# Kernel tuning notes

Hardware: AMD Instinct MI355X
Metric: run time of the kernel (lower is better)

The kernel has to match this reference:

```python
import jax, jax.numpy as jnp
import numpy as np

B, L, D, C, H, NB = 2, 2048, 256, 8, 8, 2
S = 2                        # spatial coord dim of s
E = 2 * D - (C + 1)          # id-embedding width per D*2-(C+1)
FIN = 1 + S + E + C          # z + s + id-embed + conditionals
MAXLOC = 4096
DH = (2 * D) // H            # per-head dim


def _ln(x, sc, b):
    m = x.mean(-1, keepdims=True)
    v = ((x - m) ** 2).mean(-1, keepdims=True)
    return (x - m) * jax.lax.rsqrt(v + 1e-6) * sc + b


def setup_inputs() -> dict:
    key = jax.random.key(0)
    ks = iter(jax.random.split(key, 64))
    nrm = lambda shape: jax.random.normal(next(ks), shape, jnp.float32) * 0.02
    inp = {
        "z": jax.random.normal(next(ks), (B, L), jnp.float32),
        "conditionals": jax.random.normal(next(ks), (C,), jnp.float32),
        "s": jax.random.uniform(next(ks), (L, S), jnp.float32),
        "K": jax.random.uniform(next(ks), (L, L), jnp.float32),
        "embed": nrm((MAXLOC, E)),
        "W_in1": nrm((FIN, 4 * D)), "b_in1": jnp.zeros((4 * D,), jnp.float32),
        "W_in2": nrm((4 * D, D)), "b_in2": jnp.zeros((D,), jnp.float32),
        "bias_w": jnp.ones((NB,), jnp.float32), "bias_b": jnp.zeros((NB,), jnp.float32),
        "Wq": nrm((NB, D, 2 * D)), "bq": jnp.zeros((NB, 2 * D), jnp.float32),
        "Wk": nrm((NB, D, 2 * D)), "bk": jnp.zeros((NB, 2 * D), jnp.float32),
        "Wv": nrm((NB, D, 2 * D)), "bv": jnp.zeros((NB, 2 * D), jnp.float32),
        "Wo": nrm((NB, 2 * D, D)), "bo": jnp.zeros((NB, D), jnp.float32),
        "ln1_s": jnp.ones((NB, D), jnp.float32), "ln1_b": jnp.zeros((NB, D), jnp.float32),
        "ln2_s": jnp.ones((NB, D), jnp.float32), "ln2_b": jnp.zeros((NB, D), jnp.float32),
        "Wf1": nrm((NB, D, 4 * D)), "bf1": jnp.zeros((NB, 4 * D), jnp.float32),
        "Wf2": nrm((NB, 4 * D, D)), "bf2": jnp.zeros((NB, D), jnp.float32),
        "Wh1": nrm((D, 128)), "bh1": jnp.zeros((128,), jnp.float32),
        "Wh2": nrm((128, 1)), "bh2": jnp.zeros((1,), jnp.float32),
    }
    return inp


def reference(z, conditionals, s, K, embed, W_in1, b_in1, W_in2, b_in2,
              bias_w, bias_b, Wq, bq, Wk, bk, Wv, bv, Wo, bo,
              ln1_s, ln1_b, ln2_s, ln2_b, Wf1, bf1, Wf2, bf2,
              Wh1, bh1, Wh2, bh2):
    Bx, Lx = z.shape
    ids_e = embed[:Lx]  # ids = arange(L), so embedding lookup is a leading slice
    feats = jnp.concatenate([
        z[..., None],                                          # (B, L, 1)
        jnp.broadcast_to(s[None], (Bx, Lx, S)),                # (B, L, S)
        jnp.broadcast_to(ids_e[None], (Bx, Lx, E)),            # (B, L, E)
        jnp.broadcast_to(conditionals[None, None], (Bx, Lx, C)),  # cond_as_feats
    ], axis=-1)
    x = jax.nn.gelu(feats @ W_in1 + b_in1) @ W_in2 + b_in2     # (B, L, D)
    for i in range(NB):
        bias = bias_w[i] * K + bias_b[i]                        # learned scalar-affine kernel bias (L, L)
        h = _ln(x, ln1_s[i], ln1_b[i])
        q = (h @ Wq[i] + bq[i]).reshape(Bx, Lx, H, DH)
        k = (h @ Wk[i] + bk[i]).reshape(Bx, Lx, H, DH)
        v = (h @ Wv[i] + bv[i]).reshape(Bx, Lx, H, DH)
        scores = jnp.einsum('bqhd,bkhd->bhqk', q, k) / jnp.sqrt(jnp.float32(DH))
        scores = scores + bias[None, None]                      # broadcast over batch, heads
        a = jax.nn.softmax(scores, axis=-1)
        o = jnp.einsum('bhqk,bkhd->bqhd', a, v).reshape(Bx, Lx, 2 * D)
        x = x + (o @ Wo[i] + bo[i])
        h2 = _ln(x, ln2_s[i], ln2_b[i])
        x = x + jax.nn.gelu(h2 @ Wf1[i] + bf1[i]) @ Wf2[i] + bf2[i]
    return jax.nn.gelu(x @ Wh1 + bh1) @ Wh2 + bh2              # head MLP([128,1]) -> (B, L, 1)
```

## Files before the change

kernel.cpp:

```cpp
#include <hip/hip_runtime.h>
#include <math.h>

#define B_SZ 2
#define L_LEN 2048
#define D_MOD 256
#define H_HEADS 8
#define NB_BLK 2
#define S_SZ 2
#define E_SZ 503
#define C_SZ 8
#define FIN 514
#define FIN_PAD 576
#define LOG2E 1.44269504088896340736f
#define QSC (0.125f * LOG2E)

typedef short bf16x8 __attribute__((ext_vector_type(8)));
typedef float f32x4 __attribute__((ext_vector_type(4)));
typedef unsigned short u16x4 __attribute__((ext_vector_type(4)));
typedef unsigned short u16x8 __attribute__((ext_vector_type(8)));

#define OFF_IN1 0
#define OFF_IN2 589824
#define OFF_QKV 851968
#define OFF_O   1638400
#define OFF_F1  1900544
#define OFF_F2  2424832
#define OFF_H   2949120
#define WT_END  3047424

__device__ __forceinline__ unsigned short f2bf(float x) {
    unsigned u = __float_as_uint(x);
    u += 0x7FFFu + ((u >> 16) & 1u);
    return (unsigned short)(u >> 16);
}

__device__ __forceinline__ float bf2f(unsigned short h) {
    return __uint_as_float(((unsigned)h) << 16);
}

__device__ __forceinline__ float gelu_f(float x) {
    float x3 = x * x * x;
    return 0.5f * x * (1.0f + tanhf(0.7978845608028654f * (x + 0.044715f * x3)));
}

__device__ __forceinline__ void gll16(const void* g, void* l) {
    __builtin_amdgcn_global_load_lds(
        (const __attribute__((address_space(1))) unsigned int*)g,
        (__attribute__((address_space(3))) unsigned int*)l,
        16, 0, 0);
}

__global__ __launch_bounds__(256) void prep_kernel(
    const float* __restrict__ W_in1, const float* __restrict__ W_in2,
    const float* __restrict__ Wq, const float* __restrict__ Wk,
    const float* __restrict__ Wv, const float* __restrict__ Wo,
    const float* __restrict__ Wf1, const float* __restrict__ Wf2,
    const float* __restrict__ Wh1, const float* __restrict__ Kmat,
    const float* __restrict__ bias_w,
    const float* __restrict__ bq, const float* __restrict__ bk,
    const float* __restrict__ bv,
    const float* __restrict__ z, const float* __restrict__ s,
    const float* __restrict__ embed, const float* __restrict__ cond,
    unsigned short* __restrict__ wt, unsigned short* __restrict__ kbt,
    float* __restrict__ bqkv, unsigned short* __restrict__ feats)
{
    __shared__ float sTf[64][65];
    int b = blockIdx.x;
    int t = threadIdx.x;

    if (b < 720) {
        unsigned short (*sT)[65] = (unsigned short (*)[65])&sTf[0][0];
        const float* src; unsigned short* dst; int K, N, Kp, tile;
        float scale = 1.0f;
        if (b < 144)      { src = W_in1; dst = wt + OFF_IN1; K = 514;  N = 1024; Kp = 576;  tile = b; }
        else if (b < 208) { src = W_in2; dst = wt + OFF_IN2; K = 1024; N = 256;  Kp = 1024; tile = b - 144; }
        else if (b < 400) { int t2 = b - 208;
                            int sec = t2 >> 5; tile = t2 & 31;
                            int i = sec / 3, which = sec % 3;
                            const float* wsrc = which == 0 ? Wq : which == 1 ? Wk : Wv;
                            if (which == 0) scale = QSC;
                            src = wsrc + (size_t)i * 131072;
                            dst = wt + OFF_QKV + (size_t)i * 393216 + (size_t)which * 131072;
                            K = 256; N = 512; Kp = 256; }
        else if (b < 464) { int t2 = b - 400; int i = t2 >> 5; tile = t2 & 31;
                            src = Wo + (size_t)i * 131072; dst = wt + OFF_O + (size_t)i * 131072;
                            K = 512; N = 256; Kp = 512; }
        else if (b < 592) { int t2 = b - 464; int i = t2 >> 6; tile = t2 & 63;
                            src = Wf1 + (size_t)i * 262144; dst = wt + OFF_F1 + (size_t)i * 262144;
                            K = 256; N = 1024; Kp = 256; }
        else              { int t2 = b - 592; int i = t2 >> 6; tile = t2 & 63;
                            src = Wf2 + (size_t)i * 262144; dst = wt + OFF_F2 + (size_t)i * 262144;
                            K = 1024; N = 256; Kp = 1024; }

        int nt = N >> 6;
        int kt0 = (tile / nt) << 6;
        int nt0 = (tile % nt) << 6;
        #pragma unroll
        for (int p = 0; p < 4; p++) {
            int r = p * 16 + (t >> 4);
            int c = (t & 15) * 4;
            float4 v4 = make_float4(0.f, 0.f, 0.f, 0.f);
            if (kt0 + r < K) v4 = *(const float4*)(src + (size_t)(kt0 + r) * N + nt0 + c);
            sT[r][c + 0] = f2bf(v4.x * scale);
            sT[r][c + 1] = f2bf(v4.y * scale);
            sT[r][c + 2] = f2bf(v4.z * scale);
            sT[r][c + 3] = f2bf(v4.w * scale);
        }
        __syncthreads();
        int n = t >> 2, kq = (t & 3) * 16;
        u16x8 o0, o1;
        #pragma unroll
        for (int j = 0; j < 8; j++) {
            o0[j] = sT[kq + j][n];
            o1[j] = sT[kq + 8 + j][n];
        }
        unsigned short* dp = dst + (size_t)(nt0 + n) * Kp + kt0 + kq;
        *(u16x8*)(dp) = o0;
        *(u16x8*)(dp + 8) = o1;
    } else if (b < 1104) {
        int idx = (b - 720) * 256 + t;
        if (idx < 128 * 768) {
            int n = idx / 768, kk = idx % 768;
            int kz = kk & 255;
            float v = Wh1[(size_t)kz * 128 + n];
            unsigned short hi = f2bf(v);
            wt[OFF_H + idx] = (kk < 512) ? hi : f2bf(v - bf2f(hi));
        }
    } else if (b < 2128) {
        int tile = b - 1104;
        int qt0 = (tile & 31) << 6, kt0 = (tile >> 5) << 6;
        int rr = t >> 4, cc = (t & 15) << 2;
        #pragma unroll
        for (int p = 0; p < 4; p++) {
            int qr = p * 16 + rr;
            float4 v4 = *(const float4*)(Kmat + (size_t)(qt0 + qr) * L_LEN + kt0 + cc);
            sTf[cc + 0][qr] = v4.x;
            sTf[cc + 1][qr] = v4.y;
            sTf[cc + 2][qr] = v4.z;
            sTf[cc + 3][qr] = v4.w;
        }
        __syncthreads();
        float s0 = bias_w[0] * LOG2E, s1 = bias_w[1] * LOG2E;
        int kr = t >> 2, qc = (t & 3) << 4;
        u16x8 a0, a1, b0, b1;
        #pragma unroll
        for (int j = 0; j < 8; j++) {
            float v = sTf[kr][qc + j];
            a0[j] = f2bf(v * s0); b0[j] = f2bf(v * s1);
            float v2 = sTf[kr][qc + 8 + j];
            a1[j] = f2bf(v2 * s0); b1[j] = f2bf(v2 * s1);
        }
        unsigned short* d0 = kbt + (size_t)(kt0 + kr) * L_LEN + qt0 + qc;
        *(u16x8*)d0 = a0; *(u16x8*)(d0 + 8) = a1;
        unsigned short* d1 = d0 + (size_t)L_LEN * L_LEN;
        *(u16x8*)d1 = b0; *(u16x8*)(d1 + 8) = b1;
    } else if (b < 2140) {
        int idx = (b - 2128) * 256 + t;
        if (idx < 2 * 1536) {
            int i = idx / 1536, c = idx % 1536;
            float v;
            if (c < 512)       v = bq[i * 512 + c] * QSC;
            else if (c < 1024) v = bk[i * 512 + c - 512];
            else               v = bv[i * 512 + c - 1024];
            bqkv[idx] = v;
        }
    } else {
        int idx = (b - 2140) * 256 + t;
        const int total = B_SZ * L_LEN * FIN_PAD;
        if (idx < total) {
            int f = idx % FIN_PAD;
            int row = idx / FIN_PAD;
            int l = row % L_LEN;
            float val;
            if (f == 0)                   val = z[row];
            else if (f < 1 + S_SZ)        val = s[l * S_SZ + (f - 1)];
            else if (f < 1 + S_SZ + E_SZ) val = embed[(size_t)l * E_SZ + (f - 3)];
            else if (f < FIN)             val = cond[f - (1 + S_SZ + E_SZ)];
            else                          val = 0.0f;
            feats[idx] = f2bf(val);
        }
    }
}

__global__ __launch_bounds__(256) void xsplit_kernel(
    const float* __restrict__ x, unsigned short* __restrict__ xb)
{
    int t = blockIdx.x * 256 + threadIdx.x;
    int row = t >> 5, c8 = (t & 31) * 8;
    const float* xr = x + (size_t)row * 256 + c8;
    float4 a = *(const float4*)(xr);
    float4 b4 = *(const float4*)(xr + 4);
    u16x8 hi = { f2bf(a.x), f2bf(a.y), f2bf(a.z), f2bf(a.w),
                 f2bf(b4.x), f2bf(b4.y), f2bf(b4.z), f2bf(b4.w) };
    u16x8 lo = { f2bf(a.x - bf2f(hi[0])), f2bf(a.y - bf2f(hi[1])),
                 f2bf(a.z - bf2f(hi[2])), f2bf(a.w - bf2f(hi[3])),
                 f2bf(b4.x - bf2f(hi[4])), f2bf(b4.y - bf2f(hi[5])),
                 f2bf(b4.z - bf2f(hi[6])), f2bf(b4.w - bf2f(hi[7])) };
    unsigned short* orow = xb + (size_t)row * 768;
    *(u16x8*)(orow + c8) = hi;
    *(u16x8*)(orow + 256 + c8) = lo;
    *(u16x8*)(orow + 512 + c8) = hi;
}

template<int ACT, int OMODE>
__global__ __launch_bounds__(256) void gemmW(
    const unsigned short* __restrict__ A, const unsigned short* __restrict__ Wt,
    const float* __restrict__ bias, unsigned short* __restrict__ Cb,
    unsigned short* __restrict__ Cbk, unsigned short* __restrict__ Cbv,
    int M, int N, int Kd, int lda)
{
    __shared__ unsigned short sA[2][64][64];
    __shared__ unsigned short sB[2][128][64];
    const int tid = threadIdx.x;
    const int l = tid & 63, w = tid >> 6;
    const int g = l >> 4, n16 = l & 15;
    const int wr = w >> 1, wc = w & 1;
    const int m0 = blockIdx.y * 64, n0 = blockIdx.x * 128;
    const int r8 = l >> 3;
    const int swz8 = ((l & 7) ^ r8) * 8;

    f32x4 acc[2][4];
    #pragma unroll
    for (int mi = 0; mi < 2; mi++)
        #pragma unroll
        for (int ni = 0; ni < 4; ni++)
            acc[mi][ni] = (f32x4){0.f, 0.f, 0.f, 0.f};

#define STAGEW(buf, k0)                                                         \
    do {                                                                        \
        _Pragma("unroll")                                                       \
        for (int p = 0; p < 2; p++) {                                           \
            int row = w * 16 + p * 8 + r8;                                      \
            gll16(A + (size_t)(m0 + row) * lda + (k0) + swz8,                   \
                  &sA[buf][w * 16 + p * 8][0]);                                 \
        }                                                                       \
        _Pragma("unroll")                                                       \
        for (int p = 0; p < 4; p++) {                                           \
            int row = w * 32 + p * 8 + r8;                                      \
            gll16(Wt + (size_t)(n0 + row) * Kd + (k0) + swz8,                   \
                  &sB[buf][w * 32 + p * 8][0]);                                 \
        }                                                                       \
    } while (0)

    STAGEW(0, 0);
    __syncthreads();

    int cur = 0;
    for (int k0 = 0; k0 < Kd; k0 += 64) {
        int nxt = cur ^ 1;
        if (k0 + 64 < Kd) STAGEW(nxt, k0 + 64);
        #pragma unroll
        for (int ks = 0; ks < 2; ks++) {
            bf16x8 af[2], bfr[4];
            #pragma unroll
            for (int mi = 0; mi < 2; mi++) {
                int row = wr * 32 + mi * 16 + n16;
                af[mi] = *(const bf16x8*)((const char*)&sA[cur][row][0]
                          + ((ks * 64 + g * 16) ^ ((n16 & 7) << 4)));
            }
            #pragma unroll
            for (int ni = 0; ni < 4; ni++) {
                int row = wc * 64 + ni * 16 + n16;
                bfr[ni] = *(const bf16x8*)((const char*)&sB[cur][row][0]
                          + ((ks * 64 + g * 16) ^ ((n16 & 7) << 4)));
            }
            #pragma unroll
            for (int mi = 0; mi < 2; mi++)
                #pragma unroll
                for (int ni = 0; ni < 4; ni++)
                    acc[mi][ni] = __builtin_amdgcn_mfma_f32_16x16x32_bf16(
                        af[mi], bfr[ni], acc[mi][ni], 0, 0, 0);
        }
        __syncthreads();
        cur = nxt;
    }
#undef STAGEW

    #pragma unroll
    for (int mi = 0; mi < 2; mi++) {
        #pragma unroll
        for (int ni = 0; ni < 4; ni++) {
            int col = n0 + wc * 64 + ni * 16 + n16;
            float bv = bias[col];
            #pragma unroll
            for (int r = 0; r < 4; r++) {
                int row = m0 + wr * 32 + mi * 16 + 4 * g + r;
                float val = acc[mi][ni][r] + bv;
                if (ACT == 1) val = gelu_f(val);
                if (OMODE == 1) {
                    Cb[(size_t)row * N + col] = f2bf(val);
                } else {
                    if (col < 1024) {
                        unsigned short* dst = (col < 512) ? Cb : Cbk;
                        dst[(size_t)row * 512 + (col & 511)] = f2bf(val);
                    } else {
                        Cbv[((size_t)(row >> 11) * 512 + (col - 1024)) * L_LEN + (row & (L_LEN - 1))] = f2bf(val);
                    }
                }
            }
        }
    }
}

template<int ACT, int OMODE, int BM>
__global__ __launch_bounds__(256) void gemm_bf16(
    const unsigned short* __restrict__ A, const unsigned short* __restrict__ Wt,
    const float* __restrict__ bias, float* __restrict__ Cf,
    unsigned short* __restrict__ Cb, int M, int N, int Kd, int lda)
{
    __shared__ unsigned short sA[2][BM][64];
    __shared__ unsigned short sB[2][64][64];
    const int tid = threadIdx.x;
    const int l = tid & 63, w = tid >> 6;
    const int g = l >> 4, n16 = l & 15;
    const int m0 = blockIdx.y * BM, n0 = blockIdx.x * 64;

    const int r8 = l >> 3;
    const int swz8 = ((l & 7) ^ r8) * 8;

    const int NMI = (BM == 64) ? 2 : 1;
    const int wr = w >> 1;
    const int wc = w & 1;

    f32x4 acc[2][2];
    #pragma unroll
    for (int mi = 0; mi < 2; mi++)
        #pragma unroll
        for (int ni = 0; ni < 2; ni++)
            acc[mi][ni] = (f32x4){0.f, 0.f, 0.f, 0.f};

#define STAGE(buf, k0)                                                          \
    do {                                                                        \
        if (BM == 64) {                                                         \
            _Pragma("unroll")                                                   \
            for (int p = 0; p < 2; p++) {                                       \
                int row = w * 16 + p * 8 + r8;                                  \
                gll16(A + (size_t)(m0 + row) * lda + (k0) + swz8,               \
                      &sA[buf][w * 16 + p * 8][0]);                             \
            }                                                                   \
        } else {                                                                \
            int row = w * 8 + r8;                                               \
            gll16(A + (size_t)(m0 + row) * lda + (k0) + swz8,                   \
                  &sA[buf][w * 8][0]);                                          \
        }                                                                       \
        _Pragma("unroll")                                                       \
        for (int p = 0; p < 2; p++) {                                           \
            int row = w * 16 + p * 8 + r8;                                      \
            gll16(Wt + (size_t)(n0 + row) * Kd + (k0) + swz8,                   \
                  &sB[buf][w * 16 + p * 8][0]);                                 \
        }                                                                       \
    } while (0)

    STAGE(0, 0);
    __syncthreads();

    int cur = 0;
    for (int k0 = 0; k0 < Kd; k0 += 64) {
        int nxt = cur ^ 1;
        if (k0 + 64 < Kd) STAGE(nxt, k0 + 64);
        #pragma unroll
        for (int ks = 0; ks < 2; ks++) {
            bf16x8 af[2], bfr[2];
            #pragma unroll
            for (int mi = 0; mi < NMI; mi++) {
                int row = (BM == 64) ? (wr * 32 + mi * 16 + n16) : (wr * 16 + n16);
                af[mi] = *(const bf16x8*)((const char*)&sA[cur][row][0]
                          + ((ks * 64 + g * 16) ^ ((n16 & 7) << 4)));
            }
            #pragma unroll
            for (int ni = 0; ni < 2; ni++) {
                int row = wc * 32 + ni * 16 + n16;
                bfr[ni] = *(const bf16x8*)((const char*)&sB[cur][row][0]
                          + ((ks * 64 + g * 16) ^ ((n16 & 7) << 4)));
            }
            #pragma unroll
            for (int mi = 0; mi < NMI; mi++)
                #pragma unroll
                for (int ni = 0; ni < 2; ni++)
                    acc[mi][ni] = __builtin_amdgcn_mfma_f32_16x16x32_bf16(
                        af[mi], bfr[ni], acc[mi][ni], 0, 0, 0);
        }
        __syncthreads();
        cur = nxt;
    }
#undef STAGE

    #pragma unroll
    for (int mi = 0; mi < NMI; mi++) {
        #pragma unroll
        for (int ni = 0; ni < 2; ni++) {
            int col = n0 + wc * 32 + ni * 16 + n16;
            float bv = bias[col];
            #pragma unroll
            for (int r = 0; r < 4; r++) {
                int row = (BM == 64) ? (m0 + wr * 32 + mi * 16 + 4 * g + r)
                                     : (m0 + wr * 16 + 4 * g + r);
                float val = acc[mi][ni][r] + bv;
                if (ACT == 1) val = gelu_f(val);
                if (OMODE == 0) {
                    Cf[(size_t)row * N + col] = val;
                } else if (OMODE == 1) {
                    Cb[(size_t)row * N + col] = f2bf(val);
                } else {
                    float* cp = Cf + (size_t)row * N + col;
                    *cp += val;
                }
            }
        }
    }
}

__global__ __launch_bounds__(256) void ln_bf16(
    const float* __restrict__ x, const float* __restrict__ sc,
    const float* __restrict__ bi, unsigned short* __restrict__ out)
{
    int wave = threadIdx.x >> 6, lane = threadIdx.x & 63;
    int row = blockIdx.x * 4 + wave;
    const float* xr = x + (size_t)row * D_MOD;
    float4 v = *(const float4*)(xr + lane * 4);
    float s1 = v.x + v.y + v.z + v.w;
    float s2 = v.x * v.x + v.y * v.y + v.z * v.z + v.w * v.w;
    #pragma unroll
    for (int off = 1; off < 64; off <<= 1) {
        s1 += __shfl_xor(s1, off);
        s2 += __shfl_xor(s2, off);
    }
    float mean = s1 * (1.0f / 256.0f);
    float var = s2 * (1.0f / 256.0f) - mean * mean;
    float rs = rsqrtf(var + 1e-6f);
    float4 scv = *(const float4*)(sc + lane * 4);
    float4 bv  = *(const float4*)(bi + lane * 4);
    u16x4 o4;
    o4[0] = f2bf((v.x - mean) * rs * scv.x + bv.x);
    o4[1] = f2bf((v.y - mean) * rs * scv.y + bv.y);
    o4[2] = f2bf((v.z - mean) * rs * scv.z + bv.z);
    o4[3] = f2bf((v.w - mean) * rs * scv.w + bv.w);
    *(u16x4*)(out + (size_t)row * D_MOD + lane * 4) = o4;
}

__global__ __launch_bounds__(256, 2) void attn_mfma(
    const unsigned short* __restrict__ q, const unsigned short* __restrict__ k,
    const unsigned short* __restrict__ vt, const unsigned short* __restrict__ kmt,
    unsigned short* __restrict__ o)
{
    __shared__ unsigned short sK[2][64][64];
    __shared__ unsigned short sV[2][64][64];
    __shared__ unsigned short sKmT[2][64][64];
    __shared__ unsigned short sP[4][16][72];

    const int tid = threadIdx.x;
    const int l = tid & 63, w = tid >> 6;
    const int g = l >> 4, n16 = l & 15;
    const int qblk = blockIdx.x * 64, hh = blockIdx.y, b = blockIdx.z;

    const int r8 = l >> 3;
    const int swz8 = ((l & 7) ^ r8) * 8;

    bf16x8 qf[2];
    {
        const unsigned short* qp = q + (size_t)(b * L_LEN + qblk + w * 16 + n16) * 512 + hh * 64;
        qf[0] = *(const bf16x8*)(qp + g * 8);
        qf[1] = *(const bf16x8*)(qp + 32 + g * 8);
    }
    bf16x8 onesf;
    #pragma unroll
    for (int j = 0; j < 8; j++) onesf[j] = (short)0x3F80;

    f32x4 o_acc[4];
    #pragma unroll
    for (int c = 0; c < 4; c++) o_acc[c] = (f32x4){0.f, 0.f, 0.f, 0.f};
    f32x4 l_acc = (f32x4){0.f, 0.f, 0.f, 0.f};

    const unsigned short* kbase = k + (size_t)b * L_LEN * 512 + hh * 64;
    const unsigned short* vbase = vt + ((size_t)b * 512 + hh * 64) * L_LEN;

    #pragma unroll
    for (int p = 0; p < 2; p++) {
        int row = w * 16 + p * 8 + r8;
        gll16(kbase + (size_t)row * 512 + swz8, &sK[0][w * 16 + p * 8][0]);
        gll16(vbase + (size_t)row * L_LEN + swz8, &sV[0][w * 16 + p * 8][0]);
        gll16(kmt + (size_t)row * L_LEN + qblk + swz8, &sKmT[0][w * 16 + p * 8][0]);
    }
    __syncthreads();

    int cur = 0;
    for (int kt = 0; kt < L_LEN / 64; kt++) {
        const int nb = cur ^ 1;
        const int kblk2 = (kt + 1) << 6;
        if (kt + 1 < L_LEN / 64) {
            #pragma unroll
            for (int p = 0; p < 2; p++) {
                int row = w * 16 + p * 8 + r8;
                gll16(kbase + (size_t)(kblk2 + row) * 512 + swz8, &sK[nb][w * 16 + p * 8][0]);
                gll16(vbase + (size_t)row * L_LEN + kblk2 + swz8, &sV[nb][w * 16 + p * 8][0]);
                gll16(kmt + (size_t)(kblk2 + row) * L_LEN + qblk + swz8, &sKmT[nb][w * 16 + p * 8][0]);
            }
        }
        f32x4 sacc[4];
        #pragma unroll
        for (int c = 0; c < 4; c++) {
            const char* kb_ = (const char*)&sKmT[cur][c * 16 + n16][0];
            u16x4 kmv = *(const u16x4*)(kb_ + ((32 * w + 8 * g) ^ ((n16 & 7) << 4)));
            #pragma unroll
            for (int r = 0; r < 4; r++)
                sacc[c][r] = bf2f((unsigned short)kmv[r]);
        }
        __builtin_amdgcn_s_setprio(1);
        #pragma unroll
        for (int ks = 0; ks < 2; ks++)
            #pragma unroll
            for (int c = 0; c < 4; c++) {
                int row = c * 16 + n16;
                bf16x8 kf = *(const bf16x8*)((const char*)&sK[cur][row][0]
                             + ((ks * 64 + g * 16) ^ ((n16 & 7) << 4)));
                sacc[c] = __builtin_amdgcn_mfma_f32_16x16x32_bf16(qf[ks], kf, sacc[c], 0, 0, 0);
            }
        __builtin_amdgcn_s_setprio(0);
        float p[4][4];
        #pragma unroll
        for (int r = 0; r < 4; r++)
            #pragma unroll
            for (int c = 0; c < 4; c++)
                p[r][c] = __builtin_amdgcn_exp2f(sacc[c][r]);
        #pragma unroll
        for (int r = 0; r < 4; r++)
            #pragma unroll
            for (int c = 0; c < 4; c++)
                sP[w][4 * g + r][c * 16 + n16] = f2bf(p[r][c]);
        __builtin_amdgcn_s_setprio(1);
        #pragma unroll
        for (int ks = 0; ks < 2; ks++) {
            bf16x8 pf = *(const bf16x8*)&sP[w][n16][ks * 32 + g * 8];
            l_acc = __builtin_amdgcn_mfma_f32_16x16x32_bf16(pf, onesf, l_acc, 0, 0, 0);
            #pragma unroll
            for (int c = 0; c < 4; c++) {
                int row = c * 16 + n16;
                bf16x8 vf = *(const bf16x8*)((const char*)&sV[cur][row][0]
                             + ((ks * 64 + g * 16) ^ ((n16 & 7) << 4)));
                o_acc[c] = __builtin_amdgcn_mfma_f32_16x16x32_bf16(pf, vf, o_acc[c], 0, 0, 0);
            }
        }
        __builtin_amdgcn_s_setprio(0);
        __syncthreads();
        cur = nb;
    }

    float inv[4];
    #pragma unroll
    for (int r = 0; r < 4; r++) inv[r] = 1.0f / l_acc[r];
    #pragma unroll
    for (int c = 0; c < 4; c++)
        #pragma unroll
        for (int r = 0; r < 4; r++)
            o[(size_t)(b * L_LEN + qblk + w * 16 + 4 * g + r) * 512 + hh * 64 + c * 16 + n16]
                = f2bf(o_acc[c][r] * inv[r]);
}

__global__ __launch_bounds__(256) void hsum_kernel(
    const unsigned short* __restrict__ hb, const float* __restrict__ Wh2,
    const float* __restrict__ bh2, float* __restrict__ out)
{
    int wave = threadIdx.x >> 6, lane = threadIdx.x & 63;
    int row = blockIdx.x * 4 + wave;
    unsigned v = *(const unsigned*)(hb + (size_t)row * 128 + lane * 2);
    float v0 = __uint_as_float((v & 0xFFFFu) << 16);
    float v1 = __uint_as_float(v & 0xFFFF0000u);
    float val = v0 * Wh2[lane * 2] + v1 * Wh2[lane * 2 + 1];
    #pragma unroll
    for (int off = 1; off < 64; off <<= 1)
        val += __shfl_xor(val, off);
    if (lane == 0) out[row] = val + bh2[0];
}

extern "C" void kernel_launch(void* const* d_in, const int* in_sizes, int n_in,
                              void* d_out, int out_size, void* d_ws, size_t ws_size,
                              hipStream_t stream)
{
    const float* z      = (const float*)d_in[0];
    const float* cond   = (const float*)d_in[1];
    const float* s      = (const float*)d_in[2];
    const float* Kmat   = (const float*)d_in[3];
    const float* embed  = (const float*)d_in[4];
    const float* W_in1  = (const float*)d_in[5];
    const float* b_in1  = (const float*)d_in[6];
    const float* W_in2  = (const float*)d_in[7];
    const float* b_in2  = (const float*)d_in[8];
    const float* bias_w = (const float*)d_in[9];
    const float* bias_b = (const float*)d_in[10];
    const float* Wq     = (const float*)d_in[11];
    const float* bq     = (const float*)d_in[12];
    const float* Wk     = (const float*)d_in[13];
    const float* bk     = (const float*)d_in[14];
    const float* Wv     = (const float*)d_in[15];
    const float* bv     = (const float*)d_in[16];
    const float* Wo     = (const float*)d_in[17];
    const float* bo     = (const float*)d_in[18];
    const float* ln1_s  = (const float*)d_in[19];
    const float* ln1_b  = (const float*)d_in[20];
    const float* ln2_s  = (const float*)d_in[21];
    const float* ln2_b  = (const float*)d_in[22];
    const float* Wf1    = (const float*)d_in[23];
    const float* bf1    = (const float*)d_in[24];
    const float* Wf2    = (const float*)d_in[25];
    const float* bf2    = (const float*)d_in[26];
    const float* Wh1    = (const float*)d_in[27];
    const float* bh1    = (const float*)d_in[28];
    const float* Wh2    = (const float*)d_in[29];
    const float* bh2    = (const float*)d_in[30];
    float* out = (float*)d_out;
    (void)bias_b;

    const int M = B_SZ * L_LEN;
    char* base = (char*)d_ws;
    unsigned short* feats = (unsigned short*)base;
    float* x = (float*)(base + (size_t)M * FIN_PAD * 2);
    unsigned short* h    = (unsigned short*)((char*)x + (size_t)M * D_MOD * 4);
    unsigned short* hid1 = h    + (size_t)M * D_MOD;
    unsigned short* qb   = hid1 + (size_t)M * 1024;
    unsigned short* kb2  = qb   + (size_t)M * 512;
    unsigned short* vtb  = kb2  + (size_t)M * 512;
    unsigned short* ob   = vtb  + (size_t)M * 512;
    unsigned short* wt   = ob   + (size_t)M * 512;
    float* bqkv          = (float*)(wt + WT_END);
    unsigned short* kbt  = (unsigned short*)(bqkv + 2 * 1536);

    prep_kernel<<<dim3(11356), dim3(256), 0, stream>>>(
        W_in1, W_in2, Wq, Wk, Wv, Wo, Wf1, Wf2, Wh1, Kmat, bias_w,
        bq, bk, bv, z, s, embed, cond, wt, kbt, bqkv, feats);

    gemmW<1, 1><<<dim3(8, 64), 256, 0, stream>>>(feats, wt + OFF_IN1, b_in1, hid1, nullptr, nullptr, M, 1024, FIN_PAD, FIN_PAD);
    gemm_bf16<0, 0, 32><<<dim3(4, 128), 256, 0, stream>>>(hid1, wt + OFF_IN2, b_in2, x, nullptr, M, 256, 1024, 1024);

    for (int i = 0; i < NB_BLK; i++) {
        ln_bf16<<<dim3(M / 4), 256, 0, stream>>>(x, ln1_s + i * D_MOD, ln1_b + i * D_MOD, h);
        gemmW<0, 4><<<dim3(12, 64), 256, 0, stream>>>(h, wt + OFF_QKV + (size_t)i * 393216, bqkv + i * 1536, qb, kb2, vtb, M, 1536, 256, 256);
        attn_mfma<<<dim3(L_LEN / 64, H_HEADS, B_SZ), 256, 0, stream>>>(qb, kb2, vtb, kbt + (size_t)i * L_LEN * L_LEN, ob);
        gemm_bf16<0, 2, 32><<<dim3(4, 128), 256, 0, stream>>>(ob, wt + OFF_O + (size_t)i * 131072, bo + i * D_MOD, x, nullptr, M, 256, 512, 512);
        ln_bf16<<<dim3(M / 4), 256, 0, stream>>>(x, ln2_s + i * D_MOD, ln2_b + i * D_MOD, h);
        gemmW<1, 1><<<dim3(8, 64), 256, 0, stream>>>(h, wt + OFF_F1 + (size_t)i * 262144, bf1 + i * 1024, hid1, nullptr, nullptr, M, 1024, 256, 256);
        gemm_bf16<0, 2, 32><<<dim3(4, 128), 256, 0, stream>>>(hid1, wt + OFF_F2 + (size_t)i * 262144, bf2 + i * D_MOD, x, nullptr, M, 256, 1024, 1024);
    }
    xsplit_kernel<<<dim3(512), dim3(256), 0, stream>>>(x, hid1);
    gemm_bf16<1, 1, 64><<<dim3(2, 64), 256, 0, stream>>>(hid1, wt + OFF_H, bh1, nullptr, qb, M, 128, 768, 768);
    hsum_kernel<<<dim3(M / 4), 256, 0, stream>>>(qb, Wh2, bh2, out);
}
```

Before: 247.9 us.

## Prelay kernel bias in MFMA fragment order and fuse x split into FFN GEMM

The prep kernel now writes the scaled kernel-bias matrix directly in per-thread MFMA accumulator fragment order, so the attention kernel loads it from global memory into registers (double-buffered across key tiles) instead of staging a transposed tile through LDS. This removes the sKmT shared buffer and its LDS reads, lowering LDS use and possibly raising occupancy. Separately, the last FFN down-projection GEMM gets a new output mode that adds the residual and emits the hi/lo bf16 split directly, removing the standalone xsplit kernel launch. Costs: more register pressure in attention and scattered scalar global reads in the prep stage.

```diff
diff --git a/kernel.cpp b/kernel.cpp
--- a/kernel.cpp
+++ b/kernel.cpp
@@ -61,15 +61,14 @@
     const float* __restrict__ bv,
     const float* __restrict__ z, const float* __restrict__ s,
     const float* __restrict__ embed, const float* __restrict__ cond,
-    unsigned short* __restrict__ wt, unsigned short* __restrict__ kbt,
+    unsigned short* __restrict__ wt, unsigned short* __restrict__ kmfrag,
     float* __restrict__ bqkv, unsigned short* __restrict__ feats)
 {
-    __shared__ float sTf[64][65];
+    __shared__ unsigned short sT[64][65];
     int b = blockIdx.x;
     int t = threadIdx.x;
 
     if (b < 720) {
-        unsigned short (*sT)[65] = (unsigned short (*)[65])&sTf[0][0];
         const float* src; unsigned short* dst; int K, N, Kp, tile;
         float scale = 1.0f;
         if (b < 144)      { src = W_in1; dst = wt + OFF_IN1; K = 514;  N = 1024; Kp = 576;  tile = b; }
@@ -126,36 +125,28 @@
             unsigned short hi = f2bf(v);
             wt[OFF_H + idx] = (kk < 512) ? hi : f2bf(v - bf2f(hi));
         }
-    } else if (b < 2128) {
-        int tile = b - 1104;
-        int qt0 = (tile & 31) << 6, kt0 = (tile >> 5) << 6;
-        int rr = t >> 4, cc = (t & 15) << 2;
-        #pragma unroll
-        for (int p = 0; p < 4; p++) {
-            int qr = p * 16 + rr;
-            float4 v4 = *(const float4*)(Kmat + (size_t)(qt0 + qr) * L_LEN + kt0 + cc);
-            sTf[cc + 0][qr] = v4.x;
-            sTf[cc + 1][qr] = v4.y;
-            sTf[cc + 2][qr] = v4.z;
-            sTf[cc + 3][qr] = v4.w;
-        }
-        __syncthreads();
-        float s0 = bias_w[0] * LOG2E, s1 = bias_w[1] * LOG2E;
-        int kr = t >> 2, qc = (t & 3) << 4;
-        u16x8 a0, a1, b0, b1;
-        #pragma unroll
-        for (int j = 0; j < 8; j++) {
-            float v = sTf[kr][qc + j];
-            a0[j] = f2bf(v * s0); b0[j] = f2bf(v * s1);
-            float v2 = sTf[kr][qc + 8 + j];
-            a1[j] = f2bf(v2 * s0); b1[j] = f2bf(v2 * s1);
-        }
-        unsigned short* d0 = kbt + (size_t)(kt0 + kr) * L_LEN + qt0 + qc;
-        *(u16x8*)d0 = a0; *(u16x8*)(d0 + 8) = a1;
-        unsigned short* d1 = d0 + (size_t)L_LEN * L_LEN;
-        *(u16x8*)d1 = b0; *(u16x8*)(d1 + 8) = b1;
-    } else if (b < 2140) {
-        int idx = (b - 2128) * 256 + t;
+    } else if (b < 3152) {
+        int t2 = b - 1104;
+        int i = t2 >> 10, rem = t2 & 1023;
+        int kt = rem >> 5, qb = rem & 31;
+        float sc = bias_w[i] * LOG2E;
+        int q0 = qb * 64 + ((t >> 6) << 4) + (((t >> 4) & 3) << 2);
+        int k0 = kt * 64 + (t & 15);
+        u16x8 f0, f1;
+        #pragma unroll
+        for (int c = 0; c < 4; c++)
+            #pragma unroll
+            for (int r = 0; r < 4; r++) {
+                float v = Kmat[(size_t)(q0 + r) * L_LEN + k0 + c * 16] * sc;
+                if (c < 2) f0[c * 4 + r] = f2bf(v);
+                else       f1[(c - 2) * 4 + r] = f2bf(v);
+            }
+        unsigned short* dp = kmfrag + ((size_t)i << 22)
+                           + (((size_t)(kt * 32 + qb)) * 256 + t) * 16;
+        *(u16x8*)dp = f0;
+        *(u16x8*)(dp + 8) = f1;
+    } else if (b < 3164) {
+        int idx = (b - 3152) * 256 + t;
         if (idx < 2 * 1536) {
             int i = idx / 1536, c = idx % 1536;
             float v;
@@ -165,7 +156,7 @@
             bqkv[idx] = v;
         }
     } else {
-        int idx = (b - 2140) * 256 + t;
+        int idx = (b - 3164) * 256 + t;
         const int total = B_SZ * L_LEN * FIN_PAD;
         if (idx < total) {
             int f = idx % FIN_PAD;
@@ -180,26 +171,6 @@
             feats[idx] = f2bf(val);
         }
     }
-}
-
-__global__ __launch_bounds__(256) void xsplit_kernel(
-    const float* __restrict__ x, unsigned short* __restrict__ xb)
-{
-    int t = blockIdx.x * 256 + threadIdx.x;
-    int row = t >> 5, c8 = (t & 31) * 8;
-    const float* xr = x + (size_t)row * 256 + c8;
-    float4 a = *(const float4*)(xr);
-    float4 b4 = *(const float4*)(xr + 4);
-    u16x8 hi = { f2bf(a.x), f2bf(a.y), f2bf(a.z), f2bf(a.w),
-                 f2bf(b4.x), f2bf(b4.y), f2bf(b4.z), f2bf(b4.w) };
-    u16x8 lo = { f2bf(a.x - bf2f(hi[0])), f2bf(a.y - bf2f(hi[1])),
-                 f2bf(a.z - bf2f(hi[2])), f2bf(a.w - bf2f(hi[3])),
-                 f2bf(b4.x - bf2f(hi[4])), f2bf(b4.y - bf2f(hi[5])),
-                 f2bf(b4.z - bf2f(hi[6])), f2bf(b4.w - bf2f(hi[7])) };
-    unsigned short* orow = xb + (size_t)row * 768;
-    *(u16x8*)(orow + c8) = hi;
-    *(u16x8*)(orow + 256 + c8) = lo;
-    *(u16x8*)(orow + 512 + c8) = hi;
 }
 
 template<int ACT, int OMODE>
@@ -401,9 +372,17 @@
                     Cf[(size_t)row * N + col] = val;
                 } else if (OMODE == 1) {
                     Cb[(size_t)row * N + col] = f2bf(val);
-                } else {
+                } else if (OMODE == 2) {
                     float* cp = Cf + (size_t)row * N + col;
                     *cp += val;
+                } else if (OMODE == 5) {
+                    float xnew = Cf[(size_t)row * N + col] + val;
+                    unsigned short hi = f2bf(xnew);
+                    unsigned short lo = f2bf(xnew - bf2f(hi));
+                    unsigned short* orow = Cb + (size_t)row * 768;
+                    orow[col] = hi;
+                    orow[256 + col] = lo;
+                    orow[512 + col] = hi;
                 }
             }
         }
@@ -440,12 +419,11 @@
 
 __global__ __launch_bounds__(256, 2) void attn_mfma(
     const unsigned short* __restrict__ q, const unsigned short* __restrict__ k,
-    const unsigned short* __restrict__ vt, const unsigned short* __restrict__ kmt,
+    const unsigned short* __restrict__ vt, const unsigned short* __restrict__ kmf,
     unsigned short* __restrict__ o)
 {
     __shared__ unsigned short sK[2][64][64];
     __shared__ unsigned short sV[2][64][64];
-    __shared__ unsigned short sKmT[2][64][64];
     __shared__ unsigned short sP[4][16][72];
 
     const int tid = threadIdx.x;
@@ -473,38 +451,40 @@
 
     const unsigned short* kbase = k + (size_t)b * L_LEN * 512 + hh * 64;
     const unsigned short* vbase = vt + ((size_t)b * 512 + hh * 64) * L_LEN;
+    const unsigned short* kmbase = kmf + ((size_t)blockIdx.x * 256 + tid) * 16;
 
     #pragma unroll
     for (int p = 0; p < 2; p++) {
         int row = w * 16 + p * 8 + r8;
         gll16(kbase + (size_t)row * 512 + swz8, &sK[0][w * 16 + p * 8][0]);
         gll16(vbase + (size_t)row * L_LEN + swz8, &sV[0][w * 16 + p * 8][0]);
-        gll16(kmt + (size_t)row * L_LEN + qblk + swz8, &sKmT[0][w * 16 + p * 8][0]);
-    }
+    }
+    u16x8 kmC0 = *(const u16x8*)kmbase;
+    u16x8 kmC1 = *(const u16x8*)(kmbase + 8);
     __syncthreads();
 
     int cur = 0;
     for (int kt = 0; kt < L_LEN / 64; kt++) {
         const int nb = cur ^ 1;
         const int kblk2 = (kt + 1) << 6;
+        u16x8 kmN0 = kmC0, kmN1 = kmC1;
         if (kt + 1 < L_LEN / 64) {
             #pragma unroll
             for (int p = 0; p < 2; p++) {
                 int row = w * 16 + p * 8 + r8;
                 gll16(kbase + (size_t)(kblk2 + row) * 512 + swz8, &sK[nb][w * 16 + p * 8][0]);
                 gll16(vbase + (size_t)row * L_LEN + kblk2 + swz8, &sV[nb][w * 16 + p * 8][0]);
-                gll16(kmt + (size_t)(kblk2 + row) * L_LEN + qblk + swz8, &sKmT[nb][w * 16 + p * 8][0]);
-            }
+            }
+            const unsigned short* kp2 = kmbase + (size_t)(kt + 1) * 131072;
+            kmN0 = *(const u16x8*)kp2;
+            kmN1 = *(const u16x8*)(kp2 + 8);
         }
         f32x4 sacc[4];
         #pragma unroll
-        for (int c = 0; c < 4; c++) {
-            const char* kb_ = (const char*)&sKmT[cur][c * 16 + n16][0];
-            u16x4 kmv = *(const u16x4*)(kb_ + ((32 * w + 8 * g) ^ ((n16 & 7) << 4)));
+        for (int c = 0; c < 4; c++)
             #pragma unroll
             for (int r = 0; r < 4; r++)
-                sacc[c][r] = bf2f((unsigned short)kmv[r]);
-        }
+                sacc[c][r] = bf2f((unsigned short)(c < 2 ? kmC0[c * 4 + r] : kmC1[(c - 2) * 4 + r]));
         __builtin_amdgcn_s_setprio(1);
         #pragma unroll
         for (int ks = 0; ks < 2; ks++)
@@ -543,6 +523,8 @@
         __builtin_amdgcn_s_setprio(0);
         __syncthreads();
         cur = nb;
+        kmC0 = kmN0;
+        kmC1 = kmN1;
     }
 
     float inv[4];
@@ -622,11 +604,11 @@
     unsigned short* ob   = vtb  + (size_t)M * 512;
     unsigned short* wt   = ob   + (size_t)M * 512;
     float* bqkv          = (float*)(wt + WT_END);
-    unsigned short* kbt  = (unsigned short*)(bqkv + 2 * 1536);
-
-    prep_kernel<<<dim3(11356), dim3(256), 0, stream>>>(
+    unsigned short* kmfrag = (unsigned short*)(bqkv + 2 * 1536);
+
+    prep_kernel<<<dim3(12380), dim3(256), 0, stream>>>(
         W_in1, W_in2, Wq, Wk, Wv, Wo, Wf1, Wf2, Wh1, Kmat, bias_w,
-        bq, bk, bv, z, s, embed, cond, wt, kbt, bqkv, feats);
+        bq, bk, bv, z, s, embed, cond, wt, kmfrag, bqkv, feats);
 
     gemmW<1, 1><<<dim3(8, 64), 256, 0, stream>>>(feats, wt + OFF_IN1, b_in1, hid1, nullptr, nullptr, M, 1024, FIN_PAD, FIN_PAD);
     gemm_bf16<0, 0, 32><<<dim3(4, 128), 256, 0, stream>>>(hid1, wt + OFF_IN2, b_in2, x, nullptr, M, 256, 1024, 1024);
@@ -634,13 +616,15 @@
     for (int i = 0; i < NB_BLK; i++) {
         ln_bf16<<<dim3(M / 4), 256, 0, stream>>>(x, ln1_s + i * D_MOD, ln1_b + i * D_MOD, h);
         gemmW<0, 4><<<dim3(12, 64), 256, 0, stream>>>(h, wt + OFF_QKV + (size_t)i * 393216, bqkv + i * 1536, qb, kb2, vtb, M, 1536, 256, 256);
-        attn_mfma<<<dim3(L_LEN / 64, H_HEADS, B_SZ), 256, 0, stream>>>(qb, kb2, vtb, kbt + (size_t)i * L_LEN * L_LEN, ob);
+        attn_mfma<<<dim3(L_LEN / 64, H_HEADS, B_SZ), 256, 0, stream>>>(qb, kb2, vtb, kmfrag + ((size_t)i << 22), ob);
         gemm_bf16<0, 2, 32><<<dim3(4, 128), 256, 0, stream>>>(ob, wt + OFF_O + (size_t)i * 131072, bo + i * D_MOD, x, nullptr, M, 256, 512, 512);
         ln_bf16<<<dim3(M / 4), 256, 0, stream>>>(x, ln2_s + i * D_MOD, ln2_b + i * D_MOD, h);
         gemmW<1, 1><<<dim3(8, 64), 256, 0, stream>>>(h, wt + OFF_F1 + (size_t)i * 262144, bf1 + i * 1024, hid1, nullptr, nullptr, M, 1024, 256, 256);
-        gemm_bf16<0, 2, 32><<<dim3(4, 128), 256, 0, stream>>>(hid1, wt + OFF_F2 + (size_t)i * 262144, bf2 + i * D_MOD, x, nullptr, M, 256, 1024, 1024);
-    }
-    xsplit_kernel<<<dim3(512), dim3(256), 0, stream>>>(x, hid1);
-    gemm_bf16<1, 1, 64><<<dim3(2, 64), 256, 0, stream>>>(hid1, wt + OFF_H, bh1, nullptr, qb, M, 128, 768, 768);
-    hsum_kernel<<<dim3(M / 4), 256, 0, stream>>>(qb, Wh2, bh2, out);
-}
+        if (i == 0)
+            gemm_bf16<0, 2, 32><<<dim3(4, 128), 256, 0, stream>>>(hid1, wt + OFF_F2 + (size_t)i * 262144, bf2 + i * D_MOD, x, nullptr, M, 256, 1024, 1024);
+        else
+            gemm_bf16<0, 5, 32><<<dim3(4, 128), 256, 0, stream>>>(hid1, wt + OFF_F2 + (size_t)i * 262144, bf2 + i * D_MOD, x, qb, M, 256, 1024, 1024);
+    }
+    gemm_bf16<1, 1, 64><<<dim3(2, 64), 256, 0, stream>>>(qb, wt + OFF_H, bh1, nullptr, ob, M, 128, 768, 768);
+    hsum_kernel<<<dim3(M / 4), 256, 0, stream>>>(ob, Wh2, bh2, out);
+}
```

Result: faster. 240.3 us (-3.1%).
